# Optimization experiments

Hardware: AMD Instinct MI355X
Metric: run time of the kernel (lower is better)

## Reference

```python
import jax, jax.numpy as jnp
import numpy as np

IN_F = 512
OUT_F = 512
ALPHA = 0.1  # leaky relu slope
NEG_INF = jnp.float32(-9e15)


def setup_inputs() -> dict:
    key = jax.random.key(0)
    k1, k2, k3, k4, k5 = jax.random.split(key, 5)
    bs, t = 16, 1024
    x_a = jax.random.normal(k1, (bs, t, IN_F), dtype=jnp.float32)
    x_v = jax.random.normal(k2, (bs, t, IN_F), dtype=jnp.float32)
    adj = jax.random.randint(k3, (bs, 2 * t, 2 * t), 0, 2, dtype=jnp.int32)
    # xavier_uniform with gain=1.414
    gain = 1.414
    limW = gain * np.sqrt(6.0 / (IN_F + OUT_F))
    W = jax.random.uniform(k4, (IN_F, OUT_F), minval=-limW, maxval=limW, dtype=jnp.float32)
    lima = gain * np.sqrt(6.0 / (2 * OUT_F + 1))
    a = jax.random.uniform(k5, (2 * OUT_F, 1), minval=-lima, maxval=lima, dtype=jnp.float32)
    return {"x_a": x_a, "x_v": x_v, "adj": adj, "W": W, "a": a}


def reference(x_a, x_v, adj, W, a):
    # h: (bs, 2t, in_f)
    h = jnp.concatenate([x_a, x_v], axis=1)
    Wh = jnp.matmul(h, W)                      # (bs, 2t, out_f)
    Wh1 = jnp.matmul(Wh, a[:OUT_F, :])         # (bs, 2t, 1)
    Wh2 = jnp.matmul(Wh, a[OUT_F:, :])         # (bs, 2t, 1)
    e = jax.nn.leaky_relu(Wh1 + jnp.swapaxes(Wh2, -1, -2), negative_slope=ALPHA)  # (bs, 2t, 2t)
    attention = jnp.where(adj > 0, e, NEG_INF)
    attention = jax.nn.softmax(attention, axis=-1)
    h_prime = jnp.matmul(attention, Wh)        # (bs, 2t, out_f)
    h_prime = jax.nn.elu(h_prime)
    t = x_a.shape[1]
    return h_prime[:, :t, :], h_prime[:, t:, :]
```

## Files before the change

kernel.cpp:

```cpp
#include <hip/hip_runtime.h>
#include <hip/hip_bf16.h>
#include <stdint.h>

typedef __attribute__((ext_vector_type(4))) float f32x4;
typedef __attribute__((ext_vector_type(8))) short short8;
typedef __attribute__((ext_vector_type(8))) unsigned short u16x8;
typedef __attribute__((ext_vector_type(4))) unsigned short u16x4;

__device__ __forceinline__ unsigned short f2bf(float f) {
  unsigned int u = __float_as_uint(f);
  u += 0x7fffu + ((u >> 16) & 1u);
  return (unsigned short)(u >> 16);
}
__device__ __forceinline__ float bf2f(unsigned short h) {
  return __uint_as_float(((unsigned int)h) << 16);
}

__global__ __launch_bounds__(256) void k_twp(const float* __restrict__ W,
                                             unsigned short* __restrict__ WT) {
  __shared__ float tile[64][65];
  int tid = threadIdx.x;
  int c = tid & 63, r0 = tid >> 6;
  int kb = blockIdx.x * 64, nb = blockIdx.y * 64;
#pragma unroll
  for (int rr = 0; rr < 16; ++rr) {
    int r = rr * 4 + r0;
    tile[r][c] = W[(size_t)(kb + r) * 512 + nb + c];
  }
  __syncthreads();
#pragma unroll
  for (int rr = 0; rr < 16; ++rr) {
    int r = rr * 4 + r0;
    WT[(size_t)(nb + r) * 512 + kb + c] = f2bf(tile[c][r]);
  }
}

__global__ __launch_bounds__(256) void k_gemm(const float* __restrict__ xa,
                                              const float* __restrict__ xv,
                                              const unsigned short* __restrict__ WT,
                                              unsigned short* __restrict__ WhT) {
  __shared__ __align__(16) unsigned short Al[128 * 64];
  __shared__ __align__(16) unsigned short Bl[128 * 64];
  int tid = threadIdx.x;
  int nblk = blockIdx.x;
  int mblk = blockIdx.y;
  int R0g = mblk * 128;
  int b = R0g >> 11;
  int iloc = R0g & 2047;
  const float* Abase = (iloc < 1024)
      ? (xa + ((size_t)b * 1024 + iloc) * 512)
      : (xv + ((size_t)b * 1024 + (iloc - 1024)) * 512);
  int n0 = nblk * 128;

  int lane = tid & 63;
  int wid = tid >> 6;
  int wr = wid >> 1, wc = wid & 1;

  f32x4 acc[4][4];
#pragma unroll
  for (int i = 0; i < 4; ++i) {
#pragma unroll
    for (int j = 0; j < 4; ++j) acc[i][j] = (f32x4){0.f, 0.f, 0.f, 0.f};
  }

  for (int kt = 0; kt < 8; ++kt) {
    int k0 = kt * 64;
    __syncthreads();
#pragma unroll
    for (int pass = 0; pass < 8; ++pass) {
      int gl = pass * 256 + tid;
      int row = gl >> 4;
      int gg = gl & 15;
      float4 v = *((const float4*)(Abase + (size_t)row * 512 + k0) + gg);
      u16x4 pk;
      pk.x = f2bf(v.x); pk.y = f2bf(v.y); pk.z = f2bf(v.z); pk.w = f2bf(v.w);
      int boff = (gg * 8) ^ ((row & 7) << 4);
      *(u16x4*)((char*)Al + row * 128 + boff) = pk;
    }
#pragma unroll
    for (int pass = 0; pass < 4; ++pass) {
      int gl = pass * 256 + tid;
      int row = gl >> 3;
      int g = gl & 7;
      u16x8 v = *(const u16x8*)(WT + (size_t)(n0 + row) * 512 + k0 + g * 8);
      int boff = (g * 16) ^ ((row & 7) << 4);
      *(u16x8*)((char*)Bl + row * 128 + boff) = v;
    }
    __syncthreads();
#pragma unroll
    for (int kc = 0; kc < 2; ++kc) {
      short8 af[4], bf[4];
#pragma unroll
      for (int mf = 0; mf < 4; ++mf) {
        int row = wr * 64 + mf * 16 + (lane & 15);
        int boff = ((kc * 4 + (lane >> 4)) * 16) ^ ((row & 7) << 4);
        af[mf] = *(const short8*)((const char*)Al + row * 128 + boff);
      }
#pragma unroll
      for (int nf = 0; nf < 4; ++nf) {
        int row = wc * 64 + nf * 16 + (lane & 15);
        int boff = ((kc * 4 + (lane >> 4)) * 16) ^ ((row & 7) << 4);
        bf[nf] = *(const short8*)((const char*)Bl + row * 128 + boff);
      }
#pragma unroll
      for (int mf = 0; mf < 4; ++mf) {
#pragma unroll
        for (int nf = 0; nf < 4; ++nf)
          acc[mf][nf] = __builtin_amdgcn_mfma_f32_16x16x32_bf16(af[mf], bf[nf], acc[mf][nf], 0, 0, 0);
      }
    }
  }
#pragma unroll
  for (int mf = 0; mf < 4; ++mf) {
    int jrow = iloc + wr * 64 + mf * 16 + ((lane >> 4) << 2);
#pragma unroll
    for (int nf = 0; nf < 4; ++nf) {
      int n = n0 + wc * 64 + nf * 16 + (lane & 15);
      u16x4 pk;
#pragma unroll
      for (int e = 0; e < 4; ++e) pk[e] = f2bf(acc[mf][nf][e]);
      *(u16x4*)(WhT + ((size_t)b * 512 + n) * 2048 + jrow) = pk;
    }
  }
}

__global__ __launch_bounds__(256) void k_s(const unsigned short* __restrict__ WhT,
                                           const float* __restrict__ a,
                                           float* __restrict__ s1, float* __restrict__ s2,
                                           float* __restrict__ f1, float* __restrict__ f2) {
  __shared__ float a1l[512], a2l[512];
  __shared__ float p1[256], p2[256];
  int tid = threadIdx.x;
  int b = blockIdx.y;
#pragma unroll
  for (int i = 0; i < 2; ++i) {
    a1l[tid + i * 256] = a[tid + i * 256];
    a2l[tid + i * 256] = a[512 + tid + i * 256];
  }
  __syncthreads();
  int j = blockIdx.x * 128 + (tid & 127);
  int nh = tid >> 7;
  const unsigned short* base = WhT + ((size_t)b * 512 + nh * 256) * 2048 + j;
  float c1 = 0.f, c2 = 0.f;
#pragma unroll 8
  for (int n = 0; n < 256; ++n) {
    float w = bf2f(base[(size_t)n * 2048]);
    c1 += w * a1l[nh * 256 + n];
    c2 += w * a2l[nh * 256 + n];
  }
  p1[tid] = c1; p2[tid] = c2;
  __syncthreads();
  if (tid < 128) {
    float v1 = p1[tid] + p1[tid + 128];
    float v2 = p2[tid] + p2[tid + 128];
    size_t o = (size_t)b * 2048 + j;
    s1[o] = v1; s2[o] = v2;
    f1[o] = __expf(v2);
    f2[o] = __expf(0.1f * v2);
  }
}

__global__ __launch_bounds__(512) void k_attn(const int* __restrict__ adj,
                                              const unsigned short* __restrict__ WhT,
                                              const float* __restrict__ s1g,
                                              const float* __restrict__ s2g,
                                              const float* __restrict__ f1g,
                                              const float* __restrict__ f2g,
                                              float* __restrict__ out) {
  __shared__ __align__(16) unsigned short Pl[128 * 64];
  __shared__ __align__(16) unsigned short Bl[512 * 64];
  __shared__ float s2l[2048];
  __shared__ float f1l[2048];
  __shared__ float f2l[2048];
  __shared__ float zl[128];
  __shared__ float red[8];
  int tid = threadIdx.x;
  int bx = blockIdx.x;
  int q = bx >> 3, xcd = bx & 7;
  int b = xcd * 2 + (q & 1);
  int rb = q >> 1;
  int R0 = rb * 128;

  int lane = tid & 63;
  int wid = tid >> 6;

  float lm = -1e30f;
#pragma unroll
  for (int i = 0; i < 4; ++i) {
    int idx = i * 512 + tid;
    float v = s2g[(size_t)b * 2048 + idx];
    s2l[idx] = v;
    f1l[idx] = f1g[(size_t)b * 2048 + idx];
    f2l[idx] = f2g[(size_t)b * 2048 + idx];
    lm = fmaxf(lm, v);
  }
#pragma unroll
  for (int s = 1; s < 64; s <<= 1) lm = fmaxf(lm, __shfl_xor(lm, s));
  if (lane == 0) red[wid] = lm;
  __syncthreads();
  float gmax = red[0];
#pragma unroll
  for (int i = 1; i < 8; ++i) gmax = fmaxf(gmax, red[i]);

  int r = tid >> 2;
  int qc = tid & 3;
  float s1r = s1g[(size_t)b * 2048 + R0 + r];
  float t0 = s1r + gmax;
  float M = (t0 > 0.f) ? t0 : 0.1f * t0;
  float E1 = __expf(s1r - M);
  float E2 = __expf(0.1f * s1r - M);
  float zacc = 0.f;

  f32x4 acc[4][8];
#pragma unroll
  for (int i = 0; i < 4; ++i) {
#pragma unroll
    for (int j = 0; j < 8; ++j) acc[i][j] = (f32x4){0.f, 0.f, 0.f, 0.f};
  }

  int wr2 = wid >> 2, wc = wid & 3;
  const int* adjbase = adj + ((size_t)b * 2048 + R0 + r) * 2048 + qc * 16;
  const unsigned short* whbase = WhT + (size_t)b * 512 * 2048;

  for (int jt = 0; jt < 32; ++jt) {
    int j0 = jt * 64;
    __syncthreads();
    {
      int4 av[4];
#pragma unroll
      for (int u = 0; u < 4; ++u) av[u] = *(const int4*)(adjbase + j0 + u * 4);
      const int* avs = (const int*)av;
#pragma unroll
      for (int half = 0; half < 2; ++half) {
        u16x8 pk;
#pragma unroll
        for (int c = 0; c < 8; ++c) {
          int cc = half * 8 + c;
          int jl = j0 + qc * 16 + cc;
          float t = s1r + s2l[jl];
          bool pos = t > 0.f;
          float Ev = pos ? E1 : E2;
          float Fv = pos ? f1l[jl] : f2l[jl];
          float p = (avs[cc] > 0) ? Ev * Fv : 0.f;
          unsigned short pb = f2bf(p);
          zacc += bf2f(pb);
          pk[c] = pb;
        }
        int boff = (qc * 32 + half * 16) ^ ((r & 7) << 4);
        *(u16x8*)((char*)Pl + r * 128 + boff) = pk;
      }
    }
#pragma unroll
    for (int pass = 0; pass < 8; ++pass) {
      int n = pass * 64 + (tid >> 3);
      int g = tid & 7;
      u16x8 v = *(const u16x8*)(whbase + (size_t)n * 2048 + j0 + g * 8);
      int boff = (g * 16) ^ ((n & 7) << 4);
      *(u16x8*)((char*)Bl + n * 128 + boff) = v;
    }
    __syncthreads();
#pragma unroll
    for (int kc = 0; kc < 2; ++kc) {
      short8 af[4]; short8 bfr[8];
#pragma unroll
      for (int mf = 0; mf < 4; ++mf) {
        int row = wr2 * 64 + mf * 16 + (lane & 15);
        int boff = ((kc * 4 + (lane >> 4)) * 16) ^ ((row & 7) << 4);
        af[mf] = *(const short8*)((const char*)Pl + row * 128 + boff);
      }
#pragma unroll
      for (int nf = 0; nf < 8; ++nf) {
        int n = wc * 128 + nf * 16 + (lane & 15);
        int boff = ((kc * 4 + (lane >> 4)) * 16) ^ ((n & 7) << 4);
        bfr[nf] = *(const short8*)((const char*)Bl + n * 128 + boff);
      }
#pragma unroll
      for (int mf = 0; mf < 4; ++mf) {
#pragma unroll
        for (int nf = 0; nf < 8; ++nf)
          acc[mf][nf] = __builtin_amdgcn_mfma_f32_16x16x32_bf16(af[mf], bfr[nf], acc[mf][nf], 0, 0, 0);
      }
    }
  }
  zacc += __shfl_xor(zacc, 1);
  zacc += __shfl_xor(zacc, 2);
  if (qc == 0) zl[r] = zacc;
  __syncthreads();

  float* obase;
  if (R0 < 1024) obase = out + ((size_t)b * 1024 + R0) * 512;
  else obase = out + (size_t)8388608 + ((size_t)b * 1024 + (R0 - 1024)) * 512;
#pragma unroll
  for (int mf = 0; mf < 4; ++mf) {
    int row0 = wr2 * 64 + mf * 16 + ((lane >> 4) << 2);
    float zi[4];
#pragma unroll
    for (int e = 0; e < 4; ++e) zi[e] = 1.f / zl[row0 + e];
#pragma unroll
    for (int nf = 0; nf < 8; ++nf) {
      int n = wc * 128 + nf * 16 + (lane & 15);
#pragma unroll
      for (int e = 0; e < 4; ++e) {
        float v = acc[mf][nf][e] * zi[e];
        v = (v > 0.f) ? v : (__expf(v) - 1.f);
        obase[(size_t)(row0 + e) * 512 + n] = v;
      }
    }
  }
}

extern "C" void kernel_launch(void* const* d_in, const int* in_sizes, int n_in,
                              void* d_out, int out_size, void* d_ws, size_t ws_size,
                              hipStream_t stream) {
  (void)in_sizes; (void)n_in; (void)out_size; (void)ws_size;
  const float* x_a = (const float*)d_in[0];
  const float* x_v = (const float*)d_in[1];
  const int*   adj = (const int*)d_in[2];
  const float* W   = (const float*)d_in[3];
  const float* a   = (const float*)d_in[4];
  float* out = (float*)d_out;

  char* ws = (char*)d_ws;
  unsigned short* WT  = (unsigned short*)ws;
  unsigned short* WhT = (unsigned short*)(ws + (1u << 19));
  float* s1 = (float*)(ws + (1u << 19) + (1u << 25));
  float* s2 = s1 + 32768;
  float* f1 = s2 + 32768;
  float* f2 = f1 + 32768;

  hipLaunchKernelGGL(k_twp,  dim3(8, 8),    dim3(256), 0, stream, W, WT);
  hipLaunchKernelGGL(k_gemm, dim3(4, 256),  dim3(256), 0, stream, x_a, x_v, WT, WhT);
  hipLaunchKernelGGL(k_s,    dim3(16, 16),  dim3(256), 0, stream, WhT, a, s1, s2, f1, f2);
  hipLaunchKernelGGL(k_attn, dim3(256),     dim3(512), 0, stream, adj, WhT, s1, s2, f1, f2, out);
}
```

Baseline: 528.8 us.

## Double-buffer attention loop with direct global-to-LDS loads and retile GEMM and score kernels

The attention kernel now runs a two-stage software pipeline over 32-wide j halves. It prefetches adjacency rows a step ahead and stages WhT tiles with global_load_lds straight into swizzled LDS, so loads overlap the MFMA work. The sign test uses a precomputed exp comparison instead of reading s2 from LDS. The GEMM is retiled so each block covers 64 rows by all 512 columns, with B staged via global_load_lds, which removes the redundant x reads across N-blocks. The score kernel now uses vectorized 8-wide loads and an 8-way partial reduction. Occupancy hints are added, and LDS use per block and register pressure rise.

```diff
diff --git a/kernel.cpp b/kernel.cpp
--- a/kernel.cpp
+++ b/kernel.cpp
@@ -6,6 +6,10 @@
 typedef __attribute__((ext_vector_type(8))) short short8;
 typedef __attribute__((ext_vector_type(8))) unsigned short u16x8;
 typedef __attribute__((ext_vector_type(4))) unsigned short u16x4;
+
+typedef __attribute__((address_space(1))) const unsigned int as1_u32;
+typedef __attribute__((address_space(3))) unsigned int as3_u32;
+#define GLD16(src, dst) __builtin_amdgcn_global_load_lds((as1_u32*)(src), (as3_u32*)(dst), 16, 0, 0)
 
 __device__ __forceinline__ unsigned short f2bf(float f) {
   unsigned int u = __float_as_uint(f);
@@ -35,87 +39,77 @@
   }
 }
 
-__global__ __launch_bounds__(256) void k_gemm(const float* __restrict__ xa,
-                                              const float* __restrict__ xv,
-                                              const unsigned short* __restrict__ WT,
-                                              unsigned short* __restrict__ WhT) {
-  __shared__ __align__(16) unsigned short Al[128 * 64];
-  __shared__ __align__(16) unsigned short Bl[128 * 64];
+__global__ __launch_bounds__(256, 2) void k_gemm(const float* __restrict__ xa,
+                                                 const float* __restrict__ xv,
+                                                 const unsigned short* __restrict__ WT,
+                                                 unsigned short* __restrict__ WhT) {
+  __shared__ __align__(16) unsigned short Al[64 * 64];
+  __shared__ __align__(16) unsigned short Bl[512 * 64];
   int tid = threadIdx.x;
-  int nblk = blockIdx.x;
-  int mblk = blockIdx.y;
-  int R0g = mblk * 128;
+  int rblk = blockIdx.x;
+  int R0g = rblk * 64;
   int b = R0g >> 11;
   int iloc = R0g & 2047;
   const float* Abase = (iloc < 1024)
       ? (xa + ((size_t)b * 1024 + iloc) * 512)
       : (xv + ((size_t)b * 1024 + (iloc - 1024)) * 512);
-  int n0 = nblk * 128;
 
   int lane = tid & 63;
   int wid = tid >> 6;
-  int wr = wid >> 1, wc = wid & 1;
-
-  f32x4 acc[4][4];
-#pragma unroll
-  for (int i = 0; i < 4; ++i) {
-#pragma unroll
-    for (int j = 0; j < 4; ++j) acc[i][j] = (f32x4){0.f, 0.f, 0.f, 0.f};
-  }
+  int wc = wid;
+
+  f32x4 acc[4][8];
+#pragma unroll
+  for (int i = 0; i < 4; ++i)
+#pragma unroll
+    for (int j = 0; j < 8; ++j) acc[i][j] = (f32x4){0.f, 0.f, 0.f, 0.f};
 
   for (int kt = 0; kt < 8; ++kt) {
     int k0 = kt * 64;
     __syncthreads();
 #pragma unroll
-    for (int pass = 0; pass < 8; ++pass) {
-      int gl = pass * 256 + tid;
-      int row = gl >> 4;
-      int gg = gl & 15;
+    for (int pass = 0; pass < 4; ++pass) {
+      int row = pass * 16 + (tid >> 4);
+      int gg = tid & 15;
       float4 v = *((const float4*)(Abase + (size_t)row * 512 + k0) + gg);
       u16x4 pk;
       pk.x = f2bf(v.x); pk.y = f2bf(v.y); pk.z = f2bf(v.z); pk.w = f2bf(v.w);
-      int boff = (gg * 8) ^ ((row & 7) << 4);
-      *(u16x4*)((char*)Al + row * 128 + boff) = pk;
-    }
-#pragma unroll
-    for (int pass = 0; pass < 4; ++pass) {
-      int gl = pass * 256 + tid;
-      int row = gl >> 3;
-      int g = gl & 7;
-      u16x8 v = *(const u16x8*)(WT + (size_t)(n0 + row) * 512 + k0 + g * 8);
-      int boff = (g * 16) ^ ((row & 7) << 4);
-      *(u16x8*)((char*)Bl + row * 128 + boff) = v;
+      *(u16x4*)((char*)Al + row * 128 + ((gg * 8) ^ ((row & 7) << 4))) = pk;
+    }
+#pragma unroll
+    for (int pass = 0; pass < 16; ++pass) {
+      int n = pass * 32 + (tid >> 3);
+      int g = tid & 7;
+      const unsigned short* src = WT + (size_t)n * 512 + k0 + ((g ^ (n & 7)) << 3);
+      unsigned short* dst = Bl + pass * 2048 + wid * 512;
+      GLD16(src, dst);
     }
     __syncthreads();
 #pragma unroll
     for (int kc = 0; kc < 2; ++kc) {
-      short8 af[4], bf[4];
+      int u = kc * 4 + (lane >> 4);
+      short8 af[4];
 #pragma unroll
       for (int mf = 0; mf < 4; ++mf) {
-        int row = wr * 64 + mf * 16 + (lane & 15);
-        int boff = ((kc * 4 + (lane >> 4)) * 16) ^ ((row & 7) << 4);
-        af[mf] = *(const short8*)((const char*)Al + row * 128 + boff);
+        int row = mf * 16 + (lane & 15);
+        af[mf] = *(const short8*)((const char*)Al + row * 128 + (((u ^ (row & 7)) & 7) << 4));
       }
 #pragma unroll
-      for (int nf = 0; nf < 4; ++nf) {
-        int row = wc * 64 + nf * 16 + (lane & 15);
-        int boff = ((kc * 4 + (lane >> 4)) * 16) ^ ((row & 7) << 4);
-        bf[nf] = *(const short8*)((const char*)Bl + row * 128 + boff);
+      for (int nf = 0; nf < 8; ++nf) {
+        int n = wc * 128 + nf * 16 + (lane & 15);
+        short8 bv = *(const short8*)((const char*)Bl + n * 128 + (((u ^ (n & 7)) & 7) << 4));
+#pragma unroll
+        for (int mf = 0; mf < 4; ++mf)
+          acc[mf][nf] = __builtin_amdgcn_mfma_f32_16x16x32_bf16(af[mf], bv, acc[mf][nf], 0, 0, 0);
       }
-#pragma unroll
-      for (int mf = 0; mf < 4; ++mf) {
-#pragma unroll
-        for (int nf = 0; nf < 4; ++nf)
-          acc[mf][nf] = __builtin_amdgcn_mfma_f32_16x16x32_bf16(af[mf], bf[nf], acc[mf][nf], 0, 0, 0);
-      }
     }
   }
 #pragma unroll
   for (int mf = 0; mf < 4; ++mf) {
-    int jrow = iloc + wr * 64 + mf * 16 + ((lane >> 4) << 2);
-#pragma unroll
-    for (int nf = 0; nf < 4; ++nf) {
-      int n = n0 + wc * 64 + nf * 16 + (lane & 15);
+    int jrow = iloc + mf * 16 + ((lane >> 4) << 2);
+#pragma unroll
+    for (int nf = 0; nf < 8; ++nf) {
+      int n = wc * 128 + nf * 16 + (lane & 15);
       u16x4 pk;
 #pragma unroll
       for (int e = 0; e < 4; ++e) pk[e] = f2bf(acc[mf][nf][e]);
@@ -129,49 +123,52 @@
                                            float* __restrict__ s1, float* __restrict__ s2,
                                            float* __restrict__ f1, float* __restrict__ f2) {
   __shared__ float a1l[512], a2l[512];
-  __shared__ float p1[256], p2[256];
+  __shared__ float S1p[8][256], S2p[8][256];
   int tid = threadIdx.x;
   int b = blockIdx.y;
-#pragma unroll
-  for (int i = 0; i < 2; ++i) {
-    a1l[tid + i * 256] = a[tid + i * 256];
-    a2l[tid + i * 256] = a[512 + tid + i * 256];
-  }
-  __syncthreads();
-  int j = blockIdx.x * 128 + (tid & 127);
-  int nh = tid >> 7;
-  const unsigned short* base = WhT + ((size_t)b * 512 + nh * 256) * 2048 + j;
-  float c1 = 0.f, c2 = 0.f;
-#pragma unroll 8
-  for (int n = 0; n < 256; ++n) {
-    float w = bf2f(base[(size_t)n * 2048]);
-    c1 += w * a1l[nh * 256 + n];
-    c2 += w * a2l[nh * 256 + n];
-  }
-  p1[tid] = c1; p2[tid] = c2;
-  __syncthreads();
-  if (tid < 128) {
-    float v1 = p1[tid] + p1[tid + 128];
-    float v2 = p2[tid] + p2[tid + 128];
-    size_t o = (size_t)b * 2048 + j;
-    s1[o] = v1; s2[o] = v2;
-    f1[o] = __expf(v2);
-    f2[o] = __expf(0.1f * v2);
-  }
-}
-
-__global__ __launch_bounds__(512) void k_attn(const int* __restrict__ adj,
-                                              const unsigned short* __restrict__ WhT,
-                                              const float* __restrict__ s1g,
-                                              const float* __restrict__ s2g,
-                                              const float* __restrict__ f1g,
-                                              const float* __restrict__ f2g,
-                                              float* __restrict__ out) {
-  __shared__ __align__(16) unsigned short Pl[128 * 64];
-  __shared__ __align__(16) unsigned short Bl[512 * 64];
-  __shared__ float s2l[2048];
-  __shared__ float f1l[2048];
-  __shared__ float f2l[2048];
+  int j0 = blockIdx.x * 256;
+  a1l[tid] = a[tid]; a1l[256 + tid] = a[256 + tid];
+  a2l[tid] = a[512 + tid]; a2l[256 + tid] = a[768 + tid];
+  __syncthreads();
+  int jv = (tid & 31) * 8;
+  int nh = tid >> 5;
+  const unsigned short* base = WhT + ((size_t)b * 512 + nh * 64) * 2048 + j0 + jv;
+  float c1[8], c2[8];
+#pragma unroll
+  for (int e = 0; e < 8; ++e) { c1[e] = 0.f; c2[e] = 0.f; }
+#pragma unroll 4
+  for (int i = 0; i < 64; ++i) {
+    u16x8 w = *(const u16x8*)(base + (size_t)i * 2048);
+    float w1 = a1l[nh * 64 + i], w2 = a2l[nh * 64 + i];
+#pragma unroll
+    for (int e = 0; e < 8; ++e) {
+      float wv = bf2f(w[e]);
+      c1[e] += wv * w1;
+      c2[e] += wv * w2;
+    }
+  }
+#pragma unroll
+  for (int e = 0; e < 8; ++e) { S1p[nh][jv + e] = c1[e]; S2p[nh][jv + e] = c2[e]; }
+  __syncthreads();
+  float v1 = 0.f, v2 = 0.f;
+#pragma unroll
+  for (int h = 0; h < 8; ++h) { v1 += S1p[h][tid]; v2 += S2p[h][tid]; }
+  size_t o = (size_t)b * 2048 + j0 + tid;
+  s1[o] = v1; s2[o] = v2;
+  f1[o] = __expf(v2);
+  f2[o] = __expf(0.1f * v2);
+}
+
+__global__ __launch_bounds__(512, 2) void k_attn(const int* __restrict__ adj,
+                                                 const unsigned short* __restrict__ WhT,
+                                                 const float* __restrict__ s1g,
+                                                 const float* __restrict__ s2g,
+                                                 const float* __restrict__ f1g,
+                                                 const float* __restrict__ f2g,
+                                                 float* __restrict__ out) {
+  __shared__ __align__(16) unsigned short Bl[2 * 512 * 32];
+  __shared__ __align__(16) unsigned short Pl[2 * 128 * 32];
+  __shared__ float f1l[2048], f2l[2048];
   __shared__ float zl[128];
   __shared__ float red[8];
   int tid = threadIdx.x;
@@ -181,15 +178,35 @@
   int rb = q >> 1;
   int R0 = rb * 128;
 
-  int lane = tid & 63;
-  int wid = tid >> 6;
+  int lane = tid & 63, wid = tid >> 6;
+  int wr2 = wid >> 2, wc = wid & 3;
+  int r = tid >> 2, qc = tid & 3;
+
+  const unsigned short* whbase = WhT + (size_t)b * 512 * 2048;
+  const int* adjrow = adj + ((size_t)b * 2048 + R0 + r) * 2048 + qc * 8;
+
+  auto stageB = [&](int j0h, int buf) {
+#pragma unroll
+    for (int pass = 0; pass < 4; ++pass) {
+      int n = pass * 128 + (tid >> 2);
+      int g = tid & 3;
+      const unsigned short* src = whbase + (size_t)n * 2048 + j0h + ((g ^ (n & 3)) << 3);
+      unsigned short* dst = Bl + buf * 16384 + pass * 4096 + wid * 512;
+      GLD16(src, dst);
+    }
+  };
+
+  stageB(0, 0);
+  int4 aL0 = *(const int4*)(adjrow + 0);
+  int4 aL1 = *(const int4*)(adjrow + 4);
+  int4 aH0 = *(const int4*)(adjrow + 32);
+  int4 aH1 = *(const int4*)(adjrow + 36);
 
   float lm = -1e30f;
 #pragma unroll
   for (int i = 0; i < 4; ++i) {
     int idx = i * 512 + tid;
     float v = s2g[(size_t)b * 2048 + idx];
-    s2l[idx] = v;
     f1l[idx] = f1g[(size_t)b * 2048 + idx];
     f2l[idx] = f2g[(size_t)b * 2048 + idx];
     lm = fmaxf(lm, v);
@@ -202,86 +219,91 @@
 #pragma unroll
   for (int i = 1; i < 8; ++i) gmax = fmaxf(gmax, red[i]);
 
-  int r = tid >> 2;
-  int qc = tid & 3;
   float s1r = s1g[(size_t)b * 2048 + R0 + r];
-  float t0 = s1r + gmax;
-  float M = (t0 > 0.f) ? t0 : 0.1f * t0;
+  float t0v = s1r + gmax;
+  float M = (t0v > 0.f) ? t0v : 0.1f * t0v;
   float E1 = __expf(s1r - M);
   float E2 = __expf(0.1f * s1r - M);
+  float T1 = __expf(-s1r);
   float zacc = 0.f;
 
   f32x4 acc[4][8];
 #pragma unroll
-  for (int i = 0; i < 4; ++i) {
+  for (int i = 0; i < 4; ++i)
 #pragma unroll
     for (int j = 0; j < 8; ++j) acc[i][j] = (f32x4){0.f, 0.f, 0.f, 0.f};
-  }
-
-  int wr2 = wid >> 2, wc = wid & 3;
-  const int* adjbase = adj + ((size_t)b * 2048 + R0 + r) * 2048 + qc * 16;
-  const unsigned short* whbase = WhT + (size_t)b * 512 * 2048;
-
-  for (int jt = 0; jt < 32; ++jt) {
-    int j0 = jt * 64;
+
+  auto computeP = [&](int j0h, int buf, int4 a0, int4 a1) {
+    int av[8];
+    av[0] = a0.x; av[1] = a0.y; av[2] = a0.z; av[3] = a0.w;
+    av[4] = a1.x; av[5] = a1.y; av[6] = a1.z; av[7] = a1.w;
+    int jb = j0h + qc * 8;
+    float4 A1 = *(const float4*)(f1l + jb);
+    float4 B1 = *(const float4*)(f1l + jb + 4);
+    float4 A2 = *(const float4*)(f2l + jb);
+    float4 B2 = *(const float4*)(f2l + jb + 4);
+    float f1v[8] = {A1.x, A1.y, A1.z, A1.w, B1.x, B1.y, B1.z, B1.w};
+    float f2v[8] = {A2.x, A2.y, A2.z, A2.w, B2.x, B2.y, B2.z, B2.w};
+    u16x8 pk;
+#pragma unroll
+    for (int c = 0; c < 8; ++c) {
+      bool pos = f1v[c] > T1;
+      float Ev = pos ? E1 : E2;
+      float Fv = pos ? f1v[c] : f2v[c];
+      float p = (av[c] > 0) ? Ev * Fv : 0.f;
+      unsigned short pb = f2bf(p);
+      zacc += bf2f(pb);
+      pk[c] = pb;
+    }
+    *(u16x8*)((char*)(Pl + buf * 4096) + r * 64 + ((qc ^ (r & 3)) << 4)) = pk;
+  };
+
+  auto mfmaPhase = [&](int buf) {
+    const char* pb = (const char*)(Pl + buf * 4096);
+    const char* bb = (const char*)(Bl + buf * 16384);
+    int u = lane >> 4;
+    short8 af[4];
+#pragma unroll
+    for (int mf = 0; mf < 4; ++mf) {
+      int row = wr2 * 64 + mf * 16 + (lane & 15);
+      af[mf] = *(const short8*)(pb + row * 64 + ((u ^ (row & 3)) << 4));
+    }
+#pragma unroll
+    for (int nf = 0; nf < 8; ++nf) {
+      int n = wc * 128 + nf * 16 + (lane & 15);
+      short8 bv = *(const short8*)(bb + n * 64 + ((u ^ (n & 3)) << 4));
+#pragma unroll
+      for (int mf = 0; mf < 4; ++mf)
+        acc[mf][nf] = __builtin_amdgcn_mfma_f32_16x16x32_bf16(af[mf], bv, acc[mf][nf], 0, 0, 0);
+    }
+  };
+
+  __syncthreads();
+  computeP(0, 0, aL0, aL1);
+  __syncthreads();
+
+  int4 aHn0 = aH0, aHn1 = aH1, aLn0 = aL0, aLn1 = aL1;
+  for (int t = 0; t < 32; ++t) {
+    int j0 = t << 6;
+    if (t < 31) {
+      aLn0 = *(const int4*)(adjrow + j0 + 64);
+      aLn1 = *(const int4*)(adjrow + j0 + 68);
+      aHn0 = *(const int4*)(adjrow + j0 + 96);
+      aHn1 = *(const int4*)(adjrow + j0 + 100);
+    }
+    stageB(j0 + 32, 1);
+    computeP(j0 + 32, 1, aH0, aH1);
+    mfmaPhase(0);
     __syncthreads();
-    {
-      int4 av[4];
-#pragma unroll
-      for (int u = 0; u < 4; ++u) av[u] = *(const int4*)(adjbase + j0 + u * 4);
-      const int* avs = (const int*)av;
-#pragma unroll
-      for (int half = 0; half < 2; ++half) {
-        u16x8 pk;
-#pragma unroll
-        for (int c = 0; c < 8; ++c) {
-          int cc = half * 8 + c;
-          int jl = j0 + qc * 16 + cc;
-          float t = s1r + s2l[jl];
-          bool pos = t > 0.f;
-          float Ev = pos ? E1 : E2;
-          float Fv = pos ? f1l[jl] : f2l[jl];
-          float p = (avs[cc] > 0) ? Ev * Fv : 0.f;
-          unsigned short pb = f2bf(p);
-          zacc += bf2f(pb);
-          pk[c] = pb;
-        }
-        int boff = (qc * 32 + half * 16) ^ ((r & 7) << 4);
-        *(u16x8*)((char*)Pl + r * 128 + boff) = pk;
-      }
-    }
-#pragma unroll
-    for (int pass = 0; pass < 8; ++pass) {
-      int n = pass * 64 + (tid >> 3);
-      int g = tid & 7;
-      u16x8 v = *(const u16x8*)(whbase + (size_t)n * 2048 + j0 + g * 8);
-      int boff = (g * 16) ^ ((n & 7) << 4);
-      *(u16x8*)((char*)Bl + n * 128 + boff) = v;
-    }
+    if (t < 31) {
+      stageB(j0 + 64, 0);
+      computeP(j0 + 64, 0, aLn0, aLn1);
+    }
+    mfmaPhase(1);
     __syncthreads();
-#pragma unroll
-    for (int kc = 0; kc < 2; ++kc) {
-      short8 af[4]; short8 bfr[8];
-#pragma unroll
-      for (int mf = 0; mf < 4; ++mf) {
-        int row = wr2 * 64 + mf * 16 + (lane & 15);
-        int boff = ((kc * 4 + (lane >> 4)) * 16) ^ ((row & 7) << 4);
-        af[mf] = *(const short8*)((const char*)Pl + row * 128 + boff);
-      }
-#pragma unroll
-      for (int nf = 0; nf < 8; ++nf) {
-        int n = wc * 128 + nf * 16 + (lane & 15);
-        int boff = ((kc * 4 + (lane >> 4)) * 16) ^ ((n & 7) << 4);
-        bfr[nf] = *(const short8*)((const char*)Bl + n * 128 + boff);
-      }
-#pragma unroll
-      for (int mf = 0; mf < 4; ++mf) {
-#pragma unroll
-        for (int nf = 0; nf < 8; ++nf)
-          acc[mf][nf] = __builtin_amdgcn_mfma_f32_16x16x32_bf16(af[mf], bfr[nf], acc[mf][nf], 0, 0, 0);
-      }
-    }
-  }
+    aH0 = aHn0; aH1 = aHn1;
+  }
+
   zacc += __shfl_xor(zacc, 1);
   zacc += __shfl_xor(zacc, 2);
   if (qc == 0) zl[r] = zacc;
@@ -328,8 +350,8 @@
   float* f1 = s2 + 32768;
   float* f2 = f1 + 32768;
 
-  hipLaunchKernelGGL(k_twp,  dim3(8, 8),    dim3(256), 0, stream, W, WT);
-  hipLaunchKernelGGL(k_gemm, dim3(4, 256),  dim3(256), 0, stream, x_a, x_v, WT, WhT);
-  hipLaunchKernelGGL(k_s,    dim3(16, 16),  dim3(256), 0, stream, WhT, a, s1, s2, f1, f2);
-  hipLaunchKernelGGL(k_attn, dim3(256),     dim3(512), 0, stream, adj, WhT, s1, s2, f1, f2, out);
-}
+  hipLaunchKernelGGL(k_twp,  dim3(8, 8),   dim3(256), 0, stream, W, WT);
+  hipLaunchKernelGGL(k_gemm, dim3(512),    dim3(256), 0, stream, x_a, x_v, WT, WhT);
+  hipLaunchKernelGGL(k_s,    dim3(8, 16),  dim3(256), 0, stream, WhT, a, s1, s2, f1, f2);
+  hipLaunchKernelGGL(k_attn, dim3(256),    dim3(512), 0, stream, adj, WhT, s1, s2, f1, f2, out);
+}
```

New measurement: 498.3 us. 1.06x faster.
